# Performance work log

Measured on AMD Instinct MI355X. Metric: run time of the kernel, lower is better.

Reference implementation:

```python
import jax, jax.numpy as jnp
import numpy as np

NUM_HEADS = 16
THETA = 10000.0


def _rope(x, cos, sin):
    # x: [B, H, S, d_k]; cos/sin: [S, d_k//2]
    x_even = x[..., 0::2]
    x_odd = x[..., 1::2]
    out_even = x_even * cos - x_odd * sin
    out_odd = x_odd * cos + x_even * sin
    # interleave back to original even/odd layout
    return jnp.stack([out_even, out_odd], axis=-1).reshape(x.shape)


def setup_inputs() -> dict:
    key = jax.random.key(0)
    ks = jax.random.split(key, 5)
    B, S, D = 2, 2048, 1024
    std = 2.0 / (D + D)
    return {
        "x": jax.random.normal(ks[0], (B, S, D), dtype=jnp.float32),
        "w_q": jax.random.normal(ks[1], (D, D), dtype=jnp.float32) * std,
        "w_k": jax.random.normal(ks[2], (D, D), dtype=jnp.float32) * std,
        "w_v": jax.random.normal(ks[3], (D, D), dtype=jnp.float32) * std,
        "w_o": jax.random.normal(ks[4], (D, D), dtype=jnp.float32) * std,
    }


def reference(x, w_q, w_k, w_v, w_o):
    B, S, D = x.shape
    H = NUM_HEADS
    d_k = D // H

    # QKV projections: x @ W.T
    q = jnp.einsum('bsd,ed->bse', x, w_q).reshape(B, S, H, d_k).transpose(0, 2, 1, 3)
    k = jnp.einsum('bsd,ed->bse', x, w_k).reshape(B, S, H, d_k).transpose(0, 2, 1, 3)
    v = jnp.einsum('bsd,ed->bse', x, w_v).reshape(B, S, H, d_k).transpose(0, 2, 1, 3)

    # RoPE (token_positions = arange(S))
    pos = jnp.arange(S, dtype=jnp.float32)
    inv_freq = 1.0 / (THETA ** (2.0 * jnp.arange(d_k // 2, dtype=jnp.float32) / d_k))
    angles = pos[:, None] * inv_freq[None, :]  # [S, d_k//2]
    cos, sin = jnp.cos(angles), jnp.sin(angles)
    q = _rope(q, cos, sin)
    k = _rope(k, cos, sin)

    # causal attention
    scores = jnp.einsum('bhqd,bhkd->bhqk', q, k) / jnp.sqrt(jnp.float32(d_k))
    causal = jnp.tril(jnp.ones((S, S), dtype=bool))
    scores = jnp.where(causal[None, None], scores, -jnp.inf)
    attn = jax.nn.softmax(scores, axis=-1)
    out = jnp.einsum('bhqk,bhkd->bhqd', attn, v)  # [B, H, S, d_k]

    out = out.transpose(0, 2, 1, 3).reshape(B, S, D)
    return jnp.einsum('bsd,ed->bse', out, w_o)
```

## Files before the change

### kernel.cpp

```cpp
#include <hip/hip_runtime.h>

typedef unsigned short u16;
typedef unsigned int u32;
typedef short bf16x8 __attribute__((ext_vector_type(8)));
typedef float f32x4 __attribute__((ext_vector_type(4)));

#define CSC 0.18033688011112042f

__device__ __forceinline__ u16 f2bf(float f) {
    union { float f; unsigned u; } x; x.f = f;
    unsigned r = x.u + 0x7fffu + ((x.u >> 16) & 1u);
    return (u16)(r >> 16);
}
__device__ __forceinline__ float bf2f(u16 v) {
    union { unsigned u; float f; } x; x.u = ((unsigned)v) << 16;
    return x.f;
}
__device__ __forceinline__ float exp2_fast(float x) {
#if __has_builtin(__builtin_amdgcn_exp2f)
    return __builtin_amdgcn_exp2f(x);
#else
    return exp2f(x);
#endif
}
__device__ __forceinline__ void gl_lds16(const u16* g, u16* l) {
#if __has_builtin(__builtin_amdgcn_global_load_lds)
    __builtin_amdgcn_global_load_lds(
        (const __attribute__((address_space(1))) unsigned int*)g,
        (__attribute__((address_space(3))) unsigned int*)l, 16, 0, 0);
#else
    *(bf16x8*)l = *(const bf16x8*)g;
#endif
}
__device__ __forceinline__ int ileave(int x) {
    return (x < 16) ? (x << 1) : (((x - 16) << 1) | 1);
}

__global__ void cvt_all_kernel(const float* __restrict__ x, const float* __restrict__ wq,
                               const float* __restrict__ wk, const float* __restrict__ wv,
                               const float* __restrict__ wo,
                               u16* __restrict__ xb, u16* __restrict__ qkvw,
                               u16* __restrict__ ow) {
    int i = blockIdx.x * 256 + threadIdx.x;
    const float4* src;
    ushort4* dst;
    if (i < 1048576) {
        src = (const float4*)x + i;
        dst = (ushort4*)xb + i;
    } else {
        int r = i - 1048576;
        int m = r >> 18;
        int off = r & 262143;
        const float* s4 = (m == 0) ? wq : (m == 1) ? wk : (m == 2) ? wv : wo;
        u16* d = (m < 3) ? (qkvw + (size_t)m * 1048576) : ow;
        src = (const float4*)s4 + off;
        dst = (ushort4*)d + off;
    }
    float4 v = *src;
    ushort4 o;
    o.x = f2bf(v.x); o.y = f2bf(v.y); o.z = f2bf(v.z); o.w = f2bf(v.w);
    *dst = o;
}

__global__ void rope_kernel(u16* __restrict__ qb, u16* __restrict__ kb) {
    int idx = blockIdx.x * 256 + threadIdx.x;
    u16* buf;
    float scale;
    if (blockIdx.y == 0) { buf = qb; scale = CSC; } else { buf = kb; scale = 1.0f; }
    int g   = idx & 7;
    int row = idx >> 3;
    int s   = row & 2047;
    u16* p = buf + (size_t)row * 64 + g * 8;
    bf16x8 v = *(bf16x8*)p;
    bf16x8 o;
    #pragma unroll
    for (int q = 0; q < 4; ++q) {
        int i = g * 4 + q;
        float inv = exp2_fast((float)i * -0.4152410118609203f);
        float ang = (float)s * inv;
        float sn, cs;
        sincosf(ang, &sn, &cs);
        float e  = bf2f(((u16*)&v)[2 * q]);
        float od = bf2f(((u16*)&v)[2 * q + 1]);
        ((u16*)&o)[2 * q]     = f2bf((e * cs - od * sn) * scale);
        ((u16*)&o)[2 * q + 1] = f2bf((od * cs + e * sn) * scale);
    }
    *(bf16x8*)p = o;
}

__global__ __launch_bounds__(256) void gemm_qkv(const u16* __restrict__ A,
                                                const u16* __restrict__ Bw,
                                                u16* __restrict__ C, int K) {
    __shared__ __align__(16) u16 SH[8448];
    u16* As = SH;
    u16* Bs = SH + 4096;
    const int tid  = threadIdx.x;
    const int bm   = blockIdx.x * 128;
    const int bn   = blockIdx.y * 128;
    const int wave = tid >> 6, lane = tid & 63;
    const int wm   = (wave >> 1) * 64, wn = (wave & 1) * 64;
    const int l16  = lane & 15, quad = lane >> 4;
    const int mat  = bn >> 10;

    f32x4 acc[4][4];
    #pragma unroll
    for (int i = 0; i < 4; i++)
        #pragma unroll
        for (int j = 0; j < 4; j++)
            #pragma unroll
            for (int e = 0; e < 4; e++) acc[i][j][e] = 0.0f;

    const int srow = tid >> 2, scol = (tid & 3) * 8;
    const u16* gA0 = A  + (size_t)(bm + srow) * K + scol;
    const u16* gA1 = A  + (size_t)(bm + 64 + srow) * K + scol;
    const u16* gB0 = Bw + (size_t)(bn + srow) * K + scol;
    const u16* gB1 = Bw + (size_t)(bn + 64 + srow) * K + scol;
    u16* lA0 = &As[(size_t)tid * 8];
    u16* lA1 = &As[(size_t)(tid + 256) * 8];
    u16* lB0 = &Bs[(size_t)tid * 8];
    u16* lB1 = &Bs[(size_t)(tid + 256) * 8];

    for (int k0 = 0; k0 < K; k0 += 32) {
        __syncthreads();
        gl_lds16(gA0 + k0, lA0);
        gl_lds16(gA1 + k0, lA1);
        gl_lds16(gB0 + k0, lB0);
        gl_lds16(gB1 + k0, lB1);
        __syncthreads();
        bf16x8 af[4], bfr[4];
        #pragma unroll
        for (int i = 0; i < 4; i++) af[i]  = *(const bf16x8*)&As[(wm + i * 16 + l16) * 32 + quad * 8];
        #pragma unroll
        for (int j = 0; j < 4; j++) bfr[j] = *(const bf16x8*)&Bs[(wn + j * 16 + l16) * 32 + quad * 8];
        #pragma unroll
        for (int i = 0; i < 4; i++)
            #pragma unroll
            for (int j = 0; j < 4; j++)
                acc[i][j] = __builtin_amdgcn_mfma_f32_16x16x32_bf16(af[i], bfr[j], acc[i][j], 0, 0, 0);
    }

    const int b  = bm >> 11, sb = bm & 2047;
    if (mat < 2) {
        #pragma unroll
        for (int pass = 0; pass < 2; ++pass) {
            __syncthreads();
            if ((wn >> 6) == pass) {
                #pragma unroll
                for (int i = 0; i < 4; i++)
                    #pragma unroll
                    for (int j = 0; j < 4; j++)
                        #pragma unroll
                        for (int r = 0; r < 4; r++) {
                            int rl = wm + i * 16 + quad * 4 + r;
                            int cl = j * 16 + l16;
                            SH[rl * 66 + cl] = f2bf(acc[i][j][r]);
                        }
            }
            __syncthreads();
            int rl   = tid >> 1;
            int half = (tid & 1) * 32;
            int c    = (bn + pass * 64) & 1023;
            int h    = c >> 6;
            int s    = sb + rl;
            u16* dst = C + (size_t)mat * 4194304 +
                       (((size_t)(b * 16 + h) * 2048 + s) * 64) + half;
            const u16* srcp = &SH[rl * 66 + half];
            #pragma unroll
            for (int kk = 0; kk < 4; ++kk)
                *(bf16x8*)(dst + kk * 8) = *(const bf16x8*)(srcp + kk * 8);
        }
    } else {
        #pragma unroll
        for (int pass = 0; pass < 2; ++pass) {
            __syncthreads();
            if ((wn >> 6) == pass) {
                #pragma unroll
                for (int i = 0; i < 4; i++)
                    #pragma unroll
                    for (int j = 0; j < 4; j++)
                        #pragma unroll
                        for (int r = 0; r < 4; r++) {
                            int row = j * 16 + l16;
                            int ml  = wm + i * 16 + quad * 4 + r;
                            int sp  = (ml & ~31) | ileave(ml & 31);
                            SH[row * 130 + sp] = f2bf(acc[i][j][r]);
                        }
            }
            __syncthreads();
            int row = tid >> 2, seg = tid & 3;
            int cc  = (bn + pass * 64 + row) & 1023;
            int h = cc >> 6, dv = cc & 63;
            u16* dst = C + (size_t)8388608 +
                       (((size_t)(b * 16 + h) * 64 + dv) * 2048) + sb + seg * 32;
            const u16* srcp = &SH[row * 130 + seg * 32];
            #pragma unroll
            for (int kk = 0; kk < 4; ++kk)
                *(bf16x8*)(dst + kk * 8) = *(const bf16x8*)(srcp + kk * 8);
        }
    }
}

__global__ __launch_bounds__(256, 2) void gemm_out(const u16* __restrict__ A,
                                                   const u16* __restrict__ Bw,
                                                   float* __restrict__ C, int K) {
    __shared__ __align__(16) u16 As[128 * 32];
    __shared__ __align__(16) u16 Bs[64 * 32];
    const int tid  = threadIdx.x;
    const int bm   = blockIdx.x * 128;
    const int bn   = blockIdx.y * 64;
    const int wave = tid >> 6, lane = tid & 63;
    const int wm   = wave * 32;
    const int l16  = lane & 15, quad = lane >> 4;

    f32x4 acc[2][4];
    #pragma unroll
    for (int i = 0; i < 2; i++)
        #pragma unroll
        for (int j = 0; j < 4; j++)
            #pragma unroll
            for (int e = 0; e < 4; e++) acc[i][j][e] = 0.0f;

    const int srow = tid >> 2, scol = (tid & 3) * 8;
    const u16* gA0 = A  + (size_t)(bm + srow) * K + scol;
    const u16* gA1 = A  + (size_t)(bm + 64 + srow) * K + scol;
    const u16* gB0 = Bw + (size_t)(bn + srow) * K + scol;
    u16* lA0 = &As[(size_t)tid * 8];
    u16* lA1 = &As[(size_t)(tid + 256) * 8];
    u16* lB0 = &Bs[(size_t)tid * 8];

    for (int k0 = 0; k0 < K; k0 += 32) {
        __syncthreads();
        gl_lds16(gA0 + k0, lA0);
        gl_lds16(gA1 + k0, lA1);
        gl_lds16(gB0 + k0, lB0);
        __syncthreads();
        bf16x8 af[2], bfr[4];
        #pragma unroll
        for (int i = 0; i < 2; i++) af[i]  = *(const bf16x8*)&As[(wm + i * 16 + l16) * 32 + quad * 8];
        #pragma unroll
        for (int j = 0; j < 4; j++) bfr[j] = *(const bf16x8*)&Bs[(j * 16 + l16) * 32 + quad * 8];
        #pragma unroll
        for (int i = 0; i < 2; i++)
            #pragma unroll
            for (int j = 0; j < 4; j++)
                acc[i][j] = __builtin_amdgcn_mfma_f32_16x16x32_bf16(af[i], bfr[j], acc[i][j], 0, 0, 0);
    }

    #pragma unroll
    for (int i = 0; i < 2; i++)
        #pragma unroll
        for (int j = 0; j < 4; j++)
            #pragma unroll
            for (int r = 0; r < 4; r++) {
                int mr = bm + wm + i * 16 + quad * 4 + r;
                int nc = bn + j * 16 + l16;
                C[(size_t)mr * 1024 + nc] = acc[i][j][r];
            }
}

__global__ __launch_bounds__(256, 2) void attn_kernel(const u16* __restrict__ Q,
                                                      const u16* __restrict__ Kb,
                                                      const u16* __restrict__ Vt,
                                                      u16* __restrict__ Oout) {
    __shared__ __align__(16) u16 KV[2][8192];
    __shared__ __align__(16) u16 PW[4 * 1152];
    const int tid  = threadIdx.x;
    const int wave = tid >> 6, lane = tid & 63;
    const int l16  = lane & 15, quad = lane >> 4;
    const int bid  = blockIdx.x;
    const int j    = (bid >> 3) & 15;
    const int bh   = (bid & 7) * 4 + (bid >> 7);
    const int T    = 32 - j;
    const int qA0  = j * 64 + wave * 16;
    const int qB0  = (31 - j) * 64 + wave * 16;

    const u16* Qh = Q  + (size_t)bh * 2048 * 64;
    const u16* Kh = Kb + (size_t)bh * 2048 * 64;
    const u16* Vh = Vt + (size_t)bh * 64 * 2048;

    bf16x8 qAf0 = *(const bf16x8*)&Qh[(size_t)(qA0 + l16) * 64 + quad * 8];
    bf16x8 qAf1 = *(const bf16x8*)&Qh[(size_t)(qA0 + l16) * 64 + 32 + quad * 8];
    bf16x8 qBf0 = *(const bf16x8*)&Qh[(size_t)(qB0 + l16) * 64 + quad * 8];
    bf16x8 qBf1 = *(const bf16x8*)&Qh[(size_t)(qB0 + l16) * 64 + 32 + quad * 8];

    f32x4 oA[4], oB[4];
    float lsA[4], lsB[4];
    #pragma unroll
    for (int t = 0; t < 4; t++)
        #pragma unroll
        for (int e = 0; e < 4; e++) { oA[t][e] = 0.0f; oB[t][e] = 0.0f; }
    #pragma unroll
    for (int r = 0; r < 4; r++) { lsA[r] = 0.0f; lsB[r] = 0.0f; }

    const u16* gK = Kh + (size_t)(tid >> 2) * 64 + (tid & 3) * 8;
    const u16* gV = Vh + (size_t)(tid >> 2) * 2048 + (tid & 3) * 8;

    u16* pw16 = PW + wave * 1152;
    u32* pw32 = (u32*)pw16;

    auto stage = [&](int t, int buf) {
        u16* base = KV[buf];
        gl_lds16(gK + (size_t)t * 4096,      base + (size_t)tid * 8);
        gl_lds16(gK + (size_t)t * 4096 + 32, base + 2048 + (size_t)tid * 8);
        gl_lds16(gV + (size_t)t * 64,        base + 4096 + (size_t)tid * 8);
        gl_lds16(gV + (size_t)t * 64 + 32,   base + 6144 + (size_t)tid * 8);
    };

    auto side = [&](const bf16x8& q0f, const bf16x8& q1f, bf16x8* kf0, bf16x8* kf1,
                    bf16x8* vf0, bf16x8* vf1, f32x4* o, float* ls,
                    int q0, int kbase, bool diag) {
        f32x4 s[4];
        #pragma unroll
        for (int n = 0; n < 4; n++) {
            #pragma unroll
            for (int e = 0; e < 4; e++) s[n][e] = 0.0f;
            s[n] = __builtin_amdgcn_mfma_f32_16x16x32_bf16(q0f, kf0[n], s[n], 0, 0, 0);
            s[n] = __builtin_amdgcn_mfma_f32_16x16x32_bf16(q1f, kf1[n], s[n], 0, 0, 0);
        }
        float p[4][4];
        #pragma unroll
        for (int n = 0; n < 4; n++)
            #pragma unroll
            for (int r = 0; r < 4; r++) {
                float v = exp2_fast(s[n][r]);
                if (diag) {
                    int row = q0 + quad * 4 + r;
                    v = (kbase + n * 16 + l16 > row) ? 0.0f : v;
                }
                p[n][r] = v;
                ls[r] += v;
            }
        #pragma unroll
        for (int c = 0; c < 2; c++)
            #pragma unroll
            for (int r = 0; r < 4; r++)
                pw32[(quad * 4 + r) * 36 + c * 16 + l16] =
                    (u32)f2bf(p[2 * c][r]) | ((u32)f2bf(p[2 * c + 1][r]) << 16);
        asm volatile("s_waitcnt lgkmcnt(0)" ::: "memory");
        bf16x8 pf0 = *(const bf16x8*)&pw16[l16 * 72 + quad * 8];
        bf16x8 pf1 = *(const bf16x8*)&pw16[l16 * 72 + 32 + quad * 8];
        #pragma unroll
        for (int dn = 0; dn < 4; dn++) {
            o[dn] = __builtin_amdgcn_mfma_f32_16x16x32_bf16(pf0, vf0[dn], o[dn], 0, 0, 0);
            o[dn] = __builtin_amdgcn_mfma_f32_16x16x32_bf16(pf1, vf1[dn], o[dn], 0, 0, 0);
        }
    };

    stage(0, 0);
    for (int t = 0; t < T; ++t) {
        __syncthreads();
        if (t + 1 < T) stage(t + 1, (t + 1) & 1);
        const u16* B = KV[t & 1];
        bf16x8 kf0[4], kf1[4], vf0[4], vf1[4];
        #pragma unroll
        for (int n = 0; n < 4; n++) {
            int ri = (n * 16 + l16) * 32 + quad * 8;
            kf0[n] = *(const bf16x8*)&B[ri];
            kf1[n] = *(const bf16x8*)&B[2048 + ri];
            vf0[n] = *(const bf16x8*)&B[4096 + ri];
            vf1[n] = *(const bf16x8*)&B[6144 + ri];
        }
        const int kbase = t * 64;
        side(qBf0, qBf1, kf0, kf1, vf0, vf1, oB, lsB, qB0, kbase, t == T - 1);
        if (t <= j)
            side(qAf0, qAf1, kf0, kf1, vf0, vf1, oA, lsA, qA0, kbase, t == j);
    }

    #pragma unroll
    for (int off = 1; off < 16; off <<= 1)
        #pragma unroll
        for (int r = 0; r < 4; r++) {
            lsA[r] += __shfl_xor(lsA[r], off);
            lsB[r] += __shfl_xor(lsB[r], off);
        }

    const int b = bh >> 4, h = bh & 15;
    #pragma unroll
    for (int r = 0; r < 4; r++) {
        float iA = 1.0f / lsA[r];
        float iB = 1.0f / lsB[r];
        int sA = qA0 + quad * 4 + r;
        int sB = qB0 + quad * 4 + r;
        #pragma unroll
        for (int dn = 0; dn < 4; dn++) {
            int d = h * 64 + dn * 16 + l16;
            Oout[((size_t)b * 2048 + sA) * 1024 + d] = f2bf(oA[dn][r] * iA);
            Oout[((size_t)b * 2048 + sB) * 1024 + d] = f2bf(oB[dn][r] * iB);
        }
    }
}

extern "C" void kernel_launch(void* const* d_in, const int* in_sizes, int n_in,
                              void* d_out, int out_size, void* d_ws, size_t ws_size,
                              hipStream_t stream) {
    const float* x  = (const float*)d_in[0];
    const float* wq = (const float*)d_in[1];
    const float* wk = (const float*)d_in[2];
    const float* wv = (const float*)d_in[3];
    const float* wo = (const float*)d_in[4];
    float* out = (float*)d_out;

    const int M = 4096, D = 1024;
    u16* xb    = (u16*)d_ws;
    u16* qkvw  = xb   + (size_t)M * D;
    u16* ow    = qkvw + (size_t)3 * D * D;
    u16* qkv   = ow   + (size_t)D * D;
    u16* qb    = qkv;
    u16* kb    = qkv + (size_t)M * D;
    u16* vtb   = qkv + (size_t)2 * M * D;
    u16* aob   = qkv + (size_t)3 * M * D;

    cvt_all_kernel<<<8192, 256, 0, stream>>>(x, wq, wk, wv, wo, xb, qkvw, ow);

    dim3 gq(32, 24);
    gemm_qkv<<<gq, 256, 0, stream>>>(xb, qkvw, qkv, D);

    dim3 gr(2048, 2);
    rope_kernel<<<gr, 256, 0, stream>>>(qb, kb);

    attn_kernel<<<512, 256, 0, stream>>>(qb, kb, vtb, aob);

    dim3 go(32, 16);
    gemm_out<<<go, 256, 0, stream>>>(aob, ow, out, D);
}
```

Baseline: 198.9 us.

## Split attention keys across waves with register-prefetched K/V and LDS reduction

Reworks the causal attention kernel so each block owns one 64-row query tile and its four waves split the key range, each taking every fourth 32-key chunk. K/V are loaded straight from global memory into registers with double-buffered K prefetch, replacing the shared LDS staging and per-tile barriers. Partial outputs and row sums are then reduced across waves through shared memory. The grid doubles to 1024 blocks. The bf16 packing of probabilities uses a cheaper round-and-perm helper. The cost is an extra cross-wave reduction with several barriers, redundant per-wave global loads, and imbalance where the last query tiles have few chunks.

```diff
diff --git a/kernel.cpp b/kernel.cpp
--- a/kernel.cpp
+++ b/kernel.cpp
@@ -6,6 +6,7 @@
 typedef float f32x4 __attribute__((ext_vector_type(4)));
 
 #define CSC 0.18033688011112042f
+#define MFMA16 __builtin_amdgcn_mfma_f32_16x16x32_bf16
 
 __device__ __forceinline__ u16 f2bf(float f) {
     union { float f; unsigned u; } x; x.f = f;
@@ -21,6 +22,14 @@
     return __builtin_amdgcn_exp2f(x);
 #else
     return exp2f(x);
+#endif
+}
+__device__ __forceinline__ u32 pack2bf(float a, float b) {
+    union { float f; u32 u; } xa, xb; xa.f = a; xb.f = b;
+#if __has_builtin(__builtin_amdgcn_perm)
+    return __builtin_amdgcn_perm(xb.u + 0x8000u, xa.u + 0x8000u, 0x07060302u);
+#else
+    return ((xa.u + 0x8000u) >> 16) | ((xb.u + 0x8000u) & 0xffff0000u);
 #endif
 }
 __device__ __forceinline__ void gl_lds16(const u16* g, u16* l) {
@@ -136,7 +145,7 @@
         for (int i = 0; i < 4; i++)
             #pragma unroll
             for (int j = 0; j < 4; j++)
-                acc[i][j] = __builtin_amdgcn_mfma_f32_16x16x32_bf16(af[i], bfr[j], acc[i][j], 0, 0, 0);
+                acc[i][j] = MFMA16(af[i], bfr[j], acc[i][j], 0, 0, 0);
     }
 
     const int b  = bm >> 11, sb = bm & 2047;
@@ -243,7 +252,7 @@
         for (int i = 0; i < 2; i++)
             #pragma unroll
             for (int j = 0; j < 4; j++)
-                acc[i][j] = __builtin_amdgcn_mfma_f32_16x16x32_bf16(af[i], bfr[j], acc[i][j], 0, 0, 0);
+                acc[i][j] = MFMA16(af[i], bfr[j], acc[i][j], 0, 0, 0);
     }
 
     #pragma unroll
@@ -262,131 +271,154 @@
                                                       const u16* __restrict__ Kb,
                                                       const u16* __restrict__ Vt,
                                                       u16* __restrict__ Oout) {
-    __shared__ __align__(16) u16 KV[2][8192];
-    __shared__ __align__(16) u16 PW[4 * 1152];
+    __shared__ __align__(16) float SC[4096];
+    __shared__ __align__(16) u16 PW[4][16 * 36];
+    __shared__ float LS[4][64];
     const int tid  = threadIdx.x;
     const int wave = tid >> 6, lane = tid & 63;
     const int l16  = lane & 15, quad = lane >> 4;
     const int bid  = blockIdx.x;
-    const int j    = (bid >> 3) & 15;
-    const int bh   = (bid & 7) * 4 + (bid >> 7);
-    const int T    = 32 - j;
-    const int qA0  = j * 64 + wave * 16;
-    const int qB0  = (31 - j) * 64 + wave * 16;
+    const int c    = bid & 7;
+    const int m    = bid >> 3;
+    const int bh   = (m & 3) * 8 + c;
+    const int qt   = 31 - (m >> 2);
+    const int T32  = 2 * qt + 2;
 
     const u16* Qh = Q  + (size_t)bh * 2048 * 64;
     const u16* Kh = Kb + (size_t)bh * 2048 * 64;
     const u16* Vh = Vt + (size_t)bh * 64 * 2048;
 
-    bf16x8 qAf0 = *(const bf16x8*)&Qh[(size_t)(qA0 + l16) * 64 + quad * 8];
-    bf16x8 qAf1 = *(const bf16x8*)&Qh[(size_t)(qA0 + l16) * 64 + 32 + quad * 8];
-    bf16x8 qBf0 = *(const bf16x8*)&Qh[(size_t)(qB0 + l16) * 64 + quad * 8];
-    bf16x8 qBf1 = *(const bf16x8*)&Qh[(size_t)(qB0 + l16) * 64 + 32 + quad * 8];
-
-    f32x4 oA[4], oB[4];
-    float lsA[4], lsB[4];
-    #pragma unroll
-    for (int t = 0; t < 4; t++)
-        #pragma unroll
-        for (int e = 0; e < 4; e++) { oA[t][e] = 0.0f; oB[t][e] = 0.0f; }
-    #pragma unroll
-    for (int r = 0; r < 4; r++) { lsA[r] = 0.0f; lsB[r] = 0.0f; }
-
-    const u16* gK = Kh + (size_t)(tid >> 2) * 64 + (tid & 3) * 8;
-    const u16* gV = Vh + (size_t)(tid >> 2) * 2048 + (tid & 3) * 8;
-
-    u16* pw16 = PW + wave * 1152;
-    u32* pw32 = (u32*)pw16;
-
-    auto stage = [&](int t, int buf) {
-        u16* base = KV[buf];
-        gl_lds16(gK + (size_t)t * 4096,      base + (size_t)tid * 8);
-        gl_lds16(gK + (size_t)t * 4096 + 32, base + 2048 + (size_t)tid * 8);
-        gl_lds16(gV + (size_t)t * 64,        base + 4096 + (size_t)tid * 8);
-        gl_lds16(gV + (size_t)t * 64 + 32,   base + 6144 + (size_t)tid * 8);
+    bf16x8 qf[4][2];
+    #pragma unroll
+    for (int qg = 0; qg < 4; ++qg) {
+        const u16* qp = Qh + (size_t)(qt * 64 + qg * 16 + l16) * 64 + quad * 8;
+        qf[qg][0] = *(const bf16x8*)qp;
+        qf[qg][1] = *(const bf16x8*)(qp + 32);
+    }
+
+    f32x4 o[4][4];
+    float ls[4][4];
+    #pragma unroll
+    for (int qg = 0; qg < 4; ++qg)
+        #pragma unroll
+        for (int dn = 0; dn < 4; ++dn) {
+            #pragma unroll
+            for (int e = 0; e < 4; e++) o[qg][dn][e] = 0.0f;
+            ls[qg][dn] = 0.0f;
+        }
+
+    u32* pw32 = (u32*)PW[wave];
+    u16* pw16 = PW[wave];
+
+    auto loadK = [&](int t, bf16x8* kd) {
+        const u16* kp = Kh + (size_t)(t * 32 + l16) * 64 + quad * 8;
+        kd[0] = *(const bf16x8*)kp;
+        kd[1] = *(const bf16x8*)(kp + 32);
+        kd[2] = *(const bf16x8*)(kp + 16 * 64);
+        kd[3] = *(const bf16x8*)(kp + 16 * 64 + 32);
     };
-
-    auto side = [&](const bf16x8& q0f, const bf16x8& q1f, bf16x8* kf0, bf16x8* kf1,
-                    bf16x8* vf0, bf16x8* vf1, f32x4* o, float* ls,
-                    int q0, int kbase, bool diag) {
-        f32x4 s[4];
-        #pragma unroll
-        for (int n = 0; n < 4; n++) {
-            #pragma unroll
-            for (int e = 0; e < 4; e++) s[n][e] = 0.0f;
-            s[n] = __builtin_amdgcn_mfma_f32_16x16x32_bf16(q0f, kf0[n], s[n], 0, 0, 0);
-            s[n] = __builtin_amdgcn_mfma_f32_16x16x32_bf16(q1f, kf1[n], s[n], 0, 0, 0);
-        }
-        float p[4][4];
-        #pragma unroll
-        for (int n = 0; n < 4; n++)
-            #pragma unroll
-            for (int r = 0; r < 4; r++) {
-                float v = exp2_fast(s[n][r]);
+    auto loadV = [&](int t, bf16x8* vd) {
+        const u16* vp = Vh + (size_t)l16 * 2048 + t * 32 + quad * 8;
+        vd[0] = *(const bf16x8*)vp;
+        vd[1] = *(const bf16x8*)(vp + 16 * 2048);
+        vd[2] = *(const bf16x8*)(vp + 32 * 2048);
+        vd[3] = *(const bf16x8*)(vp + 48 * 2048);
+    };
+    auto compute = [&](int t, bf16x8* kc, bf16x8* vc) {
+        const int kbase = t * 32;
+        const bool diag = (t >= 2 * qt);
+        #pragma unroll
+        for (int qg = 0; qg < 4; ++qg) {
+            f32x4 s0 = {0.f, 0.f, 0.f, 0.f}, s1 = {0.f, 0.f, 0.f, 0.f};
+            s0 = MFMA16(qf[qg][0], kc[0], s0, 0, 0, 0);
+            s0 = MFMA16(qf[qg][1], kc[1], s0, 0, 0, 0);
+            s1 = MFMA16(qf[qg][0], kc[2], s1, 0, 0, 0);
+            s1 = MFMA16(qf[qg][1], kc[3], s1, 0, 0, 0);
+            #pragma unroll
+            for (int r = 0; r < 4; ++r) {
+                float p0 = exp2_fast(s0[r]);
+                float p1 = exp2_fast(s1[r]);
                 if (diag) {
-                    int row = q0 + quad * 4 + r;
-                    v = (kbase + n * 16 + l16 > row) ? 0.0f : v;
+                    int row = qt * 64 + qg * 16 + quad * 4 + r;
+                    p0 = (kbase + l16      > row) ? 0.0f : p0;
+                    p1 = (kbase + 16 + l16 > row) ? 0.0f : p1;
                 }
-                p[n][r] = v;
-                ls[r] += v;
-            }
-        #pragma unroll
-        for (int c = 0; c < 2; c++)
-            #pragma unroll
-            for (int r = 0; r < 4; r++)
-                pw32[(quad * 4 + r) * 36 + c * 16 + l16] =
-                    (u32)f2bf(p[2 * c][r]) | ((u32)f2bf(p[2 * c + 1][r]) << 16);
-        asm volatile("s_waitcnt lgkmcnt(0)" ::: "memory");
-        bf16x8 pf0 = *(const bf16x8*)&pw16[l16 * 72 + quad * 8];
-        bf16x8 pf1 = *(const bf16x8*)&pw16[l16 * 72 + 32 + quad * 8];
-        #pragma unroll
-        for (int dn = 0; dn < 4; dn++) {
-            o[dn] = __builtin_amdgcn_mfma_f32_16x16x32_bf16(pf0, vf0[dn], o[dn], 0, 0, 0);
-            o[dn] = __builtin_amdgcn_mfma_f32_16x16x32_bf16(pf1, vf1[dn], o[dn], 0, 0, 0);
+                ls[qg][r] += p0 + p1;
+                pw32[(quad * 4 + r) * 18 + l16] = pack2bf(p0, p1);
+            }
+            asm volatile("s_waitcnt lgkmcnt(0)" ::: "memory");
+            bf16x8 pf = *(const bf16x8*)&pw16[l16 * 36 + quad * 8];
+            #pragma unroll
+            for (int dn = 0; dn < 4; ++dn)
+                o[qg][dn] = MFMA16(pf, vc[dn], o[qg][dn], 0, 0, 0);
         }
     };
 
-    stage(0, 0);
-    for (int t = 0; t < T; ++t) {
-        __syncthreads();
-        if (t + 1 < T) stage(t + 1, (t + 1) & 1);
-        const u16* B = KV[t & 1];
-        bf16x8 kf0[4], kf1[4], vf0[4], vf1[4];
-        #pragma unroll
-        for (int n = 0; n < 4; n++) {
-            int ri = (n * 16 + l16) * 32 + quad * 8;
-            kf0[n] = *(const bf16x8*)&B[ri];
-            kf1[n] = *(const bf16x8*)&B[2048 + ri];
-            vf0[n] = *(const bf16x8*)&B[4096 + ri];
-            vf1[n] = *(const bf16x8*)&B[6144 + ri];
-        }
-        const int kbase = t * 64;
-        side(qBf0, qBf1, kf0, kf1, vf0, vf1, oB, lsB, qB0, kbase, t == T - 1);
-        if (t <= j)
-            side(qAf0, qAf1, kf0, kf1, vf0, vf1, oA, lsA, qA0, kbase, t == j);
+    int nt = (wave < T32) ? ((T32 - wave + 3) >> 2) : 0;
+    if (nt > 0) {
+        bf16x8 ka[4], kb2[4], va[4];
+        loadK(wave, ka);
+        #pragma unroll
+        for (int z = 0; z < 4; ++z) kb2[z] = ka[z];
+        int t = wave, it = 0;
+        while (true) {
+            loadV(t, va);
+            if (it + 1 < nt) loadK(t + 4, kb2);
+            compute(t, ka, va);
+            ++it; t += 4; if (it >= nt) break;
+            loadV(t, va);
+            if (it + 1 < nt) loadK(t + 4, ka);
+            compute(t, kb2, va);
+            ++it; t += 4; if (it >= nt) break;
+        }
     }
 
     #pragma unroll
     for (int off = 1; off < 16; off <<= 1)
         #pragma unroll
-        for (int r = 0; r < 4; r++) {
-            lsA[r] += __shfl_xor(lsA[r], off);
-            lsB[r] += __shfl_xor(lsB[r], off);
-        }
+        for (int qg = 0; qg < 4; ++qg)
+            #pragma unroll
+            for (int r = 0; r < 4; ++r) ls[qg][r] += __shfl_xor(ls[qg][r], off);
+    if (l16 == 0) {
+        #pragma unroll
+        for (int qg = 0; qg < 4; ++qg)
+            #pragma unroll
+            for (int r = 0; r < 4; ++r) LS[wave][qg * 16 + quad * 4 + r] = ls[qg][r];
+    }
+    __syncthreads();
+
+    f32x4 lv = {0.f, 0.f, 0.f, 0.f};
+    #pragma unroll
+    for (int s = 0; s < 4; ++s) lv += *(const f32x4*)&LS[s][wave * 16 + quad * 4];
 
     const int b = bh >> 4, h = bh & 15;
     #pragma unroll
-    for (int r = 0; r < 4; r++) {
-        float iA = 1.0f / lsA[r];
-        float iB = 1.0f / lsB[r];
-        int sA = qA0 + quad * 4 + r;
-        int sB = qB0 + quad * 4 + r;
-        #pragma unroll
-        for (int dn = 0; dn < 4; dn++) {
-            int d = h * 64 + dn * 16 + l16;
-            Oout[((size_t)b * 2048 + sA) * 1024 + d] = f2bf(oA[dn][r] * iA);
-            Oout[((size_t)b * 2048 + sB) * 1024 + d] = f2bf(oB[dn][r] * iB);
-        }
+    for (int rr = 0; rr < 4; ++rr) {
+        #pragma unroll
+        for (int dn = 0; dn < 4; ++dn)
+            *(f32x4*)&SC[wave * 1024 + dn * 256 + quad * 64 + l16 * 4] = o[rr][dn];
+        __syncthreads();
+        if (wave == rr) {
+            f32x4 osum[4];
+            #pragma unroll
+            for (int dn = 0; dn < 4; ++dn) {
+                osum[dn] = *(const f32x4*)&SC[dn * 256 + quad * 64 + l16 * 4];
+                #pragma unroll
+                for (int s = 1; s < 4; ++s)
+                    osum[dn] += *(const f32x4*)&SC[s * 1024 + dn * 256 + quad * 64 + l16 * 4];
+            }
+            #pragma unroll
+            for (int r = 0; r < 4; ++r) {
+                float inv = 1.0f / lv[r];
+                int srow = qt * 64 + rr * 16 + quad * 4 + r;
+                #pragma unroll
+                for (int dn = 0; dn < 4; ++dn) {
+                    int d = h * 64 + dn * 16 + l16;
+                    Oout[((size_t)b * 2048 + srow) * 1024 + d] = f2bf(osum[dn][r] * inv);
+                }
+            }
+        }
+        __syncthreads();
     }
 }
 
@@ -418,7 +450,7 @@
     dim3 gr(2048, 2);
     rope_kernel<<<gr, 256, 0, stream>>>(qb, kb);
 
-    attn_kernel<<<512, 256, 0, stream>>>(qb, kb, vtb, aob);
+    attn_kernel<<<1024, 256, 0, stream>>>(qb, kb, vtb, aob);
 
     dim3 go(32, 16);
     gemm_out<<<go, 256, 0, stream>>>(aob, ow, out, D);
```

Measured after the change: 216.2 us. 1.09x slower.

## Split paired-tile attention blocks into one query tile per block, load V directly

Applied to the files above, without the earlier changes.

The attention kernel stops pairing a short and a long causal query tile in one block. Each block now handles a single 64-row query tile, the grid doubles to 1024 blocks, and blocks are ordered longest-first for load balance. Only K is staged through LDS, while V fragments are read straight from global memory, which halves the LDS footprint so occupancy can rise to 4 blocks per CU. The bf16 packing of P switches to a perm-based round-half-up pack, a slightly different rounding from round-to-nearest-even. The trade-off is more total blocks, more redundant K/V traffic, and uncached global V loads on the critical path.

```diff
diff --git a/kernel.cpp b/kernel.cpp
--- a/kernel.cpp
+++ b/kernel.cpp
@@ -6,6 +6,7 @@
 typedef float f32x4 __attribute__((ext_vector_type(4)));
 
 #define CSC 0.18033688011112042f
+#define MFMA16 __builtin_amdgcn_mfma_f32_16x16x32_bf16
 
 __device__ __forceinline__ u16 f2bf(float f) {
     union { float f; unsigned u; } x; x.f = f;
@@ -21,6 +22,14 @@
     return __builtin_amdgcn_exp2f(x);
 #else
     return exp2f(x);
+#endif
+}
+__device__ __forceinline__ u32 pack2bf(float a, float b) {
+    union { float f; u32 u; } xa, xb; xa.f = a; xb.f = b;
+#if __has_builtin(__builtin_amdgcn_perm)
+    return __builtin_amdgcn_perm(xb.u + 0x8000u, xa.u + 0x8000u, 0x07060302u);
+#else
+    return ((xa.u + 0x8000u) >> 16) | ((xb.u + 0x8000u) & 0xffff0000u);
 #endif
 }
 __device__ __forceinline__ void gl_lds16(const u16* g, u16* l) {
@@ -136,7 +145,7 @@
         for (int i = 0; i < 4; i++)
             #pragma unroll
             for (int j = 0; j < 4; j++)
-                acc[i][j] = __builtin_amdgcn_mfma_f32_16x16x32_bf16(af[i], bfr[j], acc[i][j], 0, 0, 0);
+                acc[i][j] = MFMA16(af[i], bfr[j], acc[i][j], 0, 0, 0);
     }
 
     const int b  = bm >> 11, sb = bm & 2047;
@@ -243,7 +252,7 @@
         for (int i = 0; i < 2; i++)
             #pragma unroll
             for (int j = 0; j < 4; j++)
-                acc[i][j] = __builtin_amdgcn_mfma_f32_16x16x32_bf16(af[i], bfr[j], acc[i][j], 0, 0, 0);
+                acc[i][j] = MFMA16(af[i], bfr[j], acc[i][j], 0, 0, 0);
     }
 
     #pragma unroll
@@ -258,65 +267,77 @@
             }
 }
 
-__global__ __launch_bounds__(256, 2) void attn_kernel(const u16* __restrict__ Q,
+__global__ __launch_bounds__(256, 4) void attn_kernel(const u16* __restrict__ Q,
                                                       const u16* __restrict__ Kb,
                                                       const u16* __restrict__ Vt,
                                                       u16* __restrict__ Oout) {
-    __shared__ __align__(16) u16 KV[2][8192];
-    __shared__ __align__(16) u16 PW[4 * 1152];
+    __shared__ __align__(16) u16 KS[2][4096];
+    __shared__ __align__(16) u16 PW[4][16 * 72];
     const int tid  = threadIdx.x;
     const int wave = tid >> 6, lane = tid & 63;
     const int l16  = lane & 15, quad = lane >> 4;
     const int bid  = blockIdx.x;
-    const int j    = (bid >> 3) & 15;
-    const int bh   = (bid & 7) * 4 + (bid >> 7);
-    const int T    = 32 - j;
-    const int qA0  = j * 64 + wave * 16;
-    const int qB0  = (31 - j) * 64 + wave * 16;
+    const int cx   = bid & 7;
+    const int mm   = bid >> 3;
+    const int bh   = (mm & 3) * 8 + cx;
+    const int qt   = 31 - (mm >> 2);
+    const int T    = qt + 1;
+    const int q0   = qt * 64 + wave * 16;
 
     const u16* Qh = Q  + (size_t)bh * 2048 * 64;
     const u16* Kh = Kb + (size_t)bh * 2048 * 64;
     const u16* Vh = Vt + (size_t)bh * 64 * 2048;
 
-    bf16x8 qAf0 = *(const bf16x8*)&Qh[(size_t)(qA0 + l16) * 64 + quad * 8];
-    bf16x8 qAf1 = *(const bf16x8*)&Qh[(size_t)(qA0 + l16) * 64 + 32 + quad * 8];
-    bf16x8 qBf0 = *(const bf16x8*)&Qh[(size_t)(qB0 + l16) * 64 + quad * 8];
-    bf16x8 qBf1 = *(const bf16x8*)&Qh[(size_t)(qB0 + l16) * 64 + 32 + quad * 8];
-
-    f32x4 oA[4], oB[4];
-    float lsA[4], lsB[4];
-    #pragma unroll
-    for (int t = 0; t < 4; t++)
-        #pragma unroll
-        for (int e = 0; e < 4; e++) { oA[t][e] = 0.0f; oB[t][e] = 0.0f; }
-    #pragma unroll
-    for (int r = 0; r < 4; r++) { lsA[r] = 0.0f; lsB[r] = 0.0f; }
+    bf16x8 qf0 = *(const bf16x8*)&Qh[(size_t)(q0 + l16) * 64 + quad * 8];
+    bf16x8 qf1 = *(const bf16x8*)&Qh[(size_t)(q0 + l16) * 64 + 32 + quad * 8];
+
+    f32x4 o[4];
+    float ls[4];
+    #pragma unroll
+    for (int dn = 0; dn < 4; dn++)
+        #pragma unroll
+        for (int e = 0; e < 4; e++) o[dn][e] = 0.0f;
+    #pragma unroll
+    for (int r = 0; r < 4; r++) ls[r] = 0.0f;
 
     const u16* gK = Kh + (size_t)(tid >> 2) * 64 + (tid & 3) * 8;
-    const u16* gV = Vh + (size_t)(tid >> 2) * 2048 + (tid & 3) * 8;
-
-    u16* pw16 = PW + wave * 1152;
+    u16* pw16 = PW[wave];
     u32* pw32 = (u32*)pw16;
 
     auto stage = [&](int t, int buf) {
-        u16* base = KV[buf];
-        gl_lds16(gK + (size_t)t * 4096,      base + (size_t)tid * 8);
-        gl_lds16(gK + (size_t)t * 4096 + 32, base + 2048 + (size_t)tid * 8);
-        gl_lds16(gV + (size_t)t * 64,        base + 4096 + (size_t)tid * 8);
-        gl_lds16(gV + (size_t)t * 64 + 32,   base + 6144 + (size_t)tid * 8);
+        gl_lds16(gK + (size_t)t * 4096,      &KS[buf][(size_t)tid * 8]);
+        gl_lds16(gK + (size_t)t * 4096 + 32, &KS[buf][2048 + (size_t)tid * 8]);
     };
 
-    auto side = [&](const bf16x8& q0f, const bf16x8& q1f, bf16x8* kf0, bf16x8* kf1,
-                    bf16x8* vf0, bf16x8* vf1, f32x4* o, float* ls,
-                    int q0, int kbase, bool diag) {
+    stage(0, 0);
+    for (int t = 0; t < T; ++t) {
+        __syncthreads();
+        const int kbase = t * 64;
+
+        bf16x8 vf0[4], vf1[4];
+        #pragma unroll
+        for (int n = 0; n < 4; n++) {
+            const u16* vp = &Vh[(size_t)(n * 16 + l16) * 2048 + kbase + quad * 8];
+            vf0[n] = *(const bf16x8*)vp;
+            vf1[n] = *(const bf16x8*)(vp + 32);
+        }
+        asm volatile("" ::: "memory");
+        if (t + 1 < T) stage(t + 1, (t + 1) & 1);
+
+        const u16* B = KS[t & 1];
         f32x4 s[4];
         #pragma unroll
         for (int n = 0; n < 4; n++) {
+            int ri = (n * 16 + l16) * 32 + quad * 8;
+            bf16x8 kf0 = *(const bf16x8*)&B[ri];
+            bf16x8 kf1 = *(const bf16x8*)&B[2048 + ri];
             #pragma unroll
             for (int e = 0; e < 4; e++) s[n][e] = 0.0f;
-            s[n] = __builtin_amdgcn_mfma_f32_16x16x32_bf16(q0f, kf0[n], s[n], 0, 0, 0);
-            s[n] = __builtin_amdgcn_mfma_f32_16x16x32_bf16(q1f, kf1[n], s[n], 0, 0, 0);
-        }
+            s[n] = MFMA16(qf0, kf0, s[n], 0, 0, 0);
+            s[n] = MFMA16(qf1, kf1, s[n], 0, 0, 0);
+        }
+
+        const bool diag = (t == T - 1);
         float p[4][4];
         #pragma unroll
         for (int n = 0; n < 4; n++)
@@ -331,61 +352,35 @@
                 ls[r] += v;
             }
         #pragma unroll
-        for (int c = 0; c < 2; c++)
+        for (int cc = 0; cc < 2; cc++)
             #pragma unroll
             for (int r = 0; r < 4; r++)
-                pw32[(quad * 4 + r) * 36 + c * 16 + l16] =
-                    (u32)f2bf(p[2 * c][r]) | ((u32)f2bf(p[2 * c + 1][r]) << 16);
+                pw32[(quad * 4 + r) * 36 + cc * 16 + l16] =
+                    pack2bf(p[2 * cc][r], p[2 * cc + 1][r]);
         asm volatile("s_waitcnt lgkmcnt(0)" ::: "memory");
         bf16x8 pf0 = *(const bf16x8*)&pw16[l16 * 72 + quad * 8];
         bf16x8 pf1 = *(const bf16x8*)&pw16[l16 * 72 + 32 + quad * 8];
         #pragma unroll
         for (int dn = 0; dn < 4; dn++) {
-            o[dn] = __builtin_amdgcn_mfma_f32_16x16x32_bf16(pf0, vf0[dn], o[dn], 0, 0, 0);
-            o[dn] = __builtin_amdgcn_mfma_f32_16x16x32_bf16(pf1, vf1[dn], o[dn], 0, 0, 0);
-        }
-    };
-
-    stage(0, 0);
-    for (int t = 0; t < T; ++t) {
-        __syncthreads();
-        if (t + 1 < T) stage(t + 1, (t + 1) & 1);
-        const u16* B = KV[t & 1];
-        bf16x8 kf0[4], kf1[4], vf0[4], vf1[4];
-        #pragma unroll
-        for (int n = 0; n < 4; n++) {
-            int ri = (n * 16 + l16) * 32 + quad * 8;
-            kf0[n] = *(const bf16x8*)&B[ri];
-            kf1[n] = *(const bf16x8*)&B[2048 + ri];
-            vf0[n] = *(const bf16x8*)&B[4096 + ri];
-            vf1[n] = *(const bf16x8*)&B[6144 + ri];
-        }
-        const int kbase = t * 64;
-        side(qBf0, qBf1, kf0, kf1, vf0, vf1, oB, lsB, qB0, kbase, t == T - 1);
-        if (t <= j)
-            side(qAf0, qAf1, kf0, kf1, vf0, vf1, oA, lsA, qA0, kbase, t == j);
+            o[dn] = MFMA16(pf0, vf0[dn], o[dn], 0, 0, 0);
+            o[dn] = MFMA16(pf1, vf1[dn], o[dn], 0, 0, 0);
+        }
     }
 
     #pragma unroll
     for (int off = 1; off < 16; off <<= 1)
         #pragma unroll
-        for (int r = 0; r < 4; r++) {
-            lsA[r] += __shfl_xor(lsA[r], off);
-            lsB[r] += __shfl_xor(lsB[r], off);
-        }
+        for (int r = 0; r < 4; r++) ls[r] += __shfl_xor(ls[r], off);
 
     const int b = bh >> 4, h = bh & 15;
     #pragma unroll
     for (int r = 0; r < 4; r++) {
-        float iA = 1.0f / lsA[r];
-        float iB = 1.0f / lsB[r];
-        int sA = qA0 + quad * 4 + r;
-        int sB = qB0 + quad * 4 + r;
+        float inv = 1.0f / ls[r];
+        int srow = q0 + quad * 4 + r;
         #pragma unroll
         for (int dn = 0; dn < 4; dn++) {
             int d = h * 64 + dn * 16 + l16;
-            Oout[((size_t)b * 2048 + sA) * 1024 + d] = f2bf(oA[dn][r] * iA);
-            Oout[((size_t)b * 2048 + sB) * 1024 + d] = f2bf(oB[dn][r] * iB);
+            Oout[((size_t)b * 2048 + srow) * 1024 + d] = f2bf(o[dn][r] * inv);
         }
     }
 }
@@ -418,7 +413,7 @@
     dim3 gr(2048, 2);
     rope_kernel<<<gr, 256, 0, stream>>>(qb, kb);
 
-    attn_kernel<<<512, 256, 0, stream>>>(qb, kb, vtb, aob);
+    attn_kernel<<<1024, 256, 0, stream>>>(qb, kb, vtb, aob);
 
     dim3 go(32, 16);
     gemm_out<<<go, 256, 0, stream>>>(aob, ow, out, D);
```

After: 228.0 us. +14.6%, slower.
